# Optimization experiments

Measured on AMD Instinct MI355X. Metric: run time of the kernel, lower is better.

The kernel has to match this reference:

```python
import jax, jax.numpy as jnp
import numpy as np

N_NODES = 100000
N_EDGES = 3200000
INP_DIM = 128
OUT_DIM = 128


def setup_inputs() -> dict:
    key = jax.random.key(0)
    ks = jax.random.split(key, 10)
    x = jax.random.normal(ks[0], (N_NODES, INP_DIM), dtype=jnp.float32)
    edge_index = jax.random.randint(ks[1], (2, N_EDGES), 0, N_NODES, dtype=jnp.int64)
    edge_attr = jax.random.uniform(ks[2], (N_EDGES,), dtype=jnp.float32)
    # GCNConv weights (glorot-style scaling) and zero biases, per PyG defaults
    def glorot(k, fin, fout):
        s = jnp.sqrt(6.0 / (fin + fout)).astype(jnp.float32)
        return jax.random.uniform(k, (fin, fout), jnp.float32, -s, s)
    W1 = glorot(ks[3], INP_DIM, 32); b1 = jnp.zeros((32,), jnp.float32)
    W2 = glorot(ks[4], 32, 64);      b2 = jnp.zeros((64,), jnp.float32)
    W3 = glorot(ks[5], 64, OUT_DIM); b3 = jnp.zeros((OUT_DIM,), jnp.float32)
    return {"x": x, "edge_index": edge_index, "edge_attr": edge_attr,
            "W1": W1, "b1": b1, "W2": W2, "b2": b2, "W3": W3, "b3": b3}


def _gcn_norm(edge_index, edge_attr, n_nodes):
    # add self-loops with weight 1, compute symmetric normalization (PyG gcn_norm)
    loop = jnp.arange(n_nodes, dtype=edge_index.dtype)
    row = jnp.concatenate([edge_index[0], loop])  # source
    col = jnp.concatenate([edge_index[1], loop])  # target
    ew = jnp.concatenate([edge_attr, jnp.ones((n_nodes,), edge_attr.dtype)])
    deg = jax.ops.segment_sum(ew, col, num_segments=n_nodes)
    dinv = jnp.where(deg > 0, jax.lax.rsqrt(jnp.maximum(deg, 1e-30)), 0.0)
    norm = dinv[row] * ew * dinv[col]  # [E + N]
    return row, col, norm


def _gcn_conv(x, row, col, norm, W, b, n_nodes):
    h = x @ W                     # [N, Fout] small GEMM first (Fout <= Fin or cheap)
    msg = h[row] * norm[:, None]  # edge-wise gather + scale
    out = jax.ops.segment_sum(msg, col, num_segments=n_nodes)  # scatter-add
    return out + b


def reference(x, edge_index, edge_attr, W1, b1, W2, b2, W3, b3):
    n = x.shape[0]
    row, col, norm = _gcn_norm(edge_index, edge_attr, n)
    h = jax.nn.elu(_gcn_conv(x, row, col, norm, W1, b1, n))
    h = jax.nn.elu(_gcn_conv(h, row, col, norm, W2, b2, n))
    return _gcn_conv(h, row, col, norm, W3, b3, n)
```

## Files before the change

kernel.cpp:

```cpp
#include <hip/hip_runtime.h>
#include <hip/hip_bf16.h>


constexpr int N = 100000;
constexpr int E = 3200000;

constexpr int BSHIFT = 7;
constexpr int BSIZE = 128;
constexpr int NBKT = (N + BSIZE - 1) / BSIZE;

constexpr float FIX_SCALE = 16777216.0f;

constexpr int HIST_EPB = 4096;
constexpr int SC_EPB = 4096;

__device__ __forceinline__ float ldf(const void* p, int isbf, size_t i) {
    return isbf ? __bfloat162float(((const __hip_bfloat16*)p)[i])
                : ((const float*)p)[i];
}

__device__ __forceinline__ int ld_idx(const void* ei, int is64, size_t pos) {
    return is64 ? (int)((const long long*)ei)[pos] : ((const int*)ei)[pos];
}

__device__ __forceinline__ float4 bf4tof4(uint2 u) {
    float4 r;
    r.x = __uint_as_float(u.x << 16);
    r.y = __uint_as_float(u.x & 0xffff0000u);
    r.z = __uint_as_float(u.y << 16);
    r.w = __uint_as_float(u.y & 0xffff0000u);
    return r;
}
__device__ __forceinline__ unsigned short f2bf(float f) {
    unsigned u = __float_as_uint(f);
    unsigned rnd = 0x7fffu + ((u >> 16) & 1u);
    return (unsigned short)((u + rnd) >> 16);
}
__device__ __forceinline__ unsigned packbf2(float a, float b) {
    return (unsigned)f2bf(a) | ((unsigned)f2bf(b) << 16);
}
__device__ __forceinline__ uint2 f4tobf4(float4 v) {
    uint2 r;
    r.x = packbf2(v.x, v.y);
    r.y = packbf2(v.z, v.w);
    return r;
}

__global__ void k_probe(const void* ei, const void* x, int* flags, int* bkt_cnt) {
    __shared__ int bad64, bigcnt;
    int t = threadIdx.x;
    if (t == 0) { bad64 = 0; bigcnt = 0; }
    __syncthreads();
    long long v = ((const long long*)ei)[t];
    if (v < 0 || v >= (long long)N) atomicAdd(&bad64, 1);
    const unsigned short* u = (const unsigned short*)x;
    int big = 0;
    for (int i = t * 16; i < t * 16 + 16; i++) {
        int e = (u[i] >> 7) & 0xFF;
        if (e >= 133) big++;
    }
    atomicAdd(&bigcnt, big);
    for (int i = t; i < NBKT; i += 256) bkt_cnt[i] = 0;
    __syncthreads();
    if (t == 0) { flags[0] = (bad64 == 0) ? 1 : 0; flags[1] = (bigcnt < 40) ? 1 : 0; }
}

__global__ __launch_bounds__(512) void k_hist(const void* ei, const int* flags,
                                              int* bkt_cnt) {
    constexpr int EPT = HIST_EPB / 512;
    __shared__ int h[NBKT];
    int t = threadIdx.x;
    for (int i = t; i < NBKT; i += 512) h[i] = 0;
    __syncthreads();
    int is64 = flags[0];
    size_t eb = (size_t)blockIdx.x * HIST_EPB;
    int nb = (int)min((size_t)HIST_EPB, (size_t)E - eb);
    int cc[EPT];
#pragma unroll
    for (int k = 0; k < EPT; k++) {
        int idx = t + k * 512;
        cc[k] = (idx < nb) ? ld_idx(ei, is64, (size_t)E + eb + idx) : -1;
    }
#pragma unroll
    for (int k = 0; k < EPT; k++)
        if (cc[k] >= 0) atomicAdd(&h[cc[k] >> BSHIFT], 1);
    __syncthreads();
    for (int i = t; i < NBKT; i += 512) {
        int v = h[i];
        if (v) atomicAdd(&bkt_cnt[i], v);
    }
}

__global__ void k_bscan(const int* bkt_cnt, int* bkt_off, int* bkt_cur) {
    __shared__ int s[256];
    int t = threadIdx.x;
    int v[4]; int sum = 0;
#pragma unroll
    for (int j = 0; j < 4; j++) {
        int i = t * 4 + j;
        v[j] = (i < NBKT) ? bkt_cnt[i] : 0;
        sum += v[j];
    }
    s[t] = sum; __syncthreads();
    for (int st = 1; st < 256; st <<= 1) {
        int add = (t >= st) ? s[t - st] : 0;
        __syncthreads();
        s[t] += add;
        __syncthreads();
    }
    int excl = s[t] - sum;
#pragma unroll
    for (int j = 0; j < 4; j++) {
        int i = t * 4 + j;
        if (i < NBKT) { bkt_off[i] = excl; bkt_cur[i] = excl; excl += v[j]; }
    }
    if (t == 0) bkt_off[NBKT] = E;
}

__global__ __launch_bounds__(512) void k_scatter(const void* ei, const int* flags,
                                                 const void* ew, int* bkt_cur,
                                                 int2* tmp) {
    constexpr int EPT = SC_EPB / 512;
    __shared__ int h[NBKT];
    __shared__ int base_s[NBKT];
    int t = threadIdx.x;
    for (int i = t; i < NBKT; i += 512) h[i] = 0;
    __syncthreads();
    int is64 = flags[0], isbf = flags[1];
    size_t eb = (size_t)blockIdx.x * SC_EPB;
    int nb = (int)min((size_t)SC_EPB, (size_t)E - eb);
    int rr[EPT], cc[EPT]; float ww[EPT];
#pragma unroll
    for (int k = 0; k < EPT; k++) {
        int idx = t + k * 512;
        if (idx < nb) {
            size_t e = eb + idx;
            rr[k] = ld_idx(ei, is64, e);
            cc[k] = ld_idx(ei, is64, (size_t)E + e);
            ww[k] = ldf(ew, isbf, e);
        } else {
            rr[k] = 0; cc[k] = -1; ww[k] = 0.f;
        }
    }
#pragma unroll
    for (int k = 0; k < EPT; k++)
        if (cc[k] >= 0) atomicAdd(&h[cc[k] >> BSHIFT], 1);
    __syncthreads();
    for (int i = t; i < NBKT; i += 512) {
        int v = h[i];
        base_s[i] = v ? atomicAdd(&bkt_cur[i], v) : 0;
    }
    __syncthreads();
    for (int i = t; i < NBKT; i += 512) h[i] = 0;
    __syncthreads();
#pragma unroll
    for (int k = 0; k < EPT; k++) {
        if (cc[k] >= 0) {
            int b = cc[k] >> BSHIFT;
            int loc = atomicAdd(&h[b], 1);
            int pos = base_s[b] + loc;
            tmp[pos] = make_int2(rr[k] | ((cc[k] & (BSIZE - 1)) << 17),
                                 __float_as_int(ww[k]));
        }
    }
}

__global__ __launch_bounds__(256) void k_nodecnt(const int2* __restrict__ tmp,
                                                 const int* __restrict__ bkt_off,
                                                 int* __restrict__ counts,
                                                 int* __restrict__ offsets,
                                                 float* __restrict__ dinv) {
    __shared__ int cnt_s[BSIZE];
    __shared__ unsigned int wfx_s[BSIZE];
    __shared__ int sc_s[BSIZE];
    int t = threadIdx.x;
    int b = blockIdx.x;
    if (t < BSIZE) { cnt_s[t] = 0; wfx_s[t] = 0u; }
    __syncthreads();
    int s0 = bkt_off[b], s1 = bkt_off[b + 1];
    for (int p = s0 + t; p < s1; p += 256) {
        int2 ev = tmp[p];
        int c7 = (int)(((unsigned)ev.x) >> 17);
        float w = __int_as_float(ev.y);
        atomicAdd(&cnt_s[c7], 1);
        atomicAdd(&wfx_s[c7], (unsigned)__float2uint_rn(w * FIX_SCALE));
    }
    __syncthreads();
    if (t < BSIZE) sc_s[t] = cnt_s[t];
    __syncthreads();
    for (int st = 1; st < BSIZE; st <<= 1) {
        int add = (t < BSIZE && t >= st) ? sc_s[t - st] : 0;
        __syncthreads();
        if (t < BSIZE) sc_s[t] += add;
        __syncthreads();
    }
    if (t < BSIZE) {
        int node = b * BSIZE + t;
        if (node < N) {
            int c = cnt_s[t];
            offsets[node] = s0 + sc_s[t] - c;
            counts[node] = c;
            float deg = 1.0f + (float)wfx_s[t] * (1.0f / FIX_SCALE);
            dinv[node] = rsqrtf(deg);
        }
    }
}

__global__ __launch_bounds__(256) void k_fill2(const int2* __restrict__ tmp,
                                               const int* __restrict__ bkt_off,
                                               const int* __restrict__ offsets,
                                               const float* __restrict__ dinv,
                                               int2* __restrict__ epk) {
    __shared__ int lcur[BSIZE];
    int t = threadIdx.x;
    int b = blockIdx.x;
    if (t < BSIZE) {
        int node = b * BSIZE + t;
        lcur[t] = (node < N) ? offsets[node] : 0;
    }
    __syncthreads();
    int s0 = bkt_off[b], s1 = bkt_off[b + 1];
    for (int p = s0 + t; p < s1; p += 256) {
        int2 ev = tmp[p];
        unsigned px = (unsigned)ev.x;
        int r = (int)(px & 0x1FFFFu);
        int c7 = (int)(px >> 17);
        float w = __int_as_float(ev.y);
        float nr = dinv[r] * w;
        int pos = atomicAdd(&lcur[c7], 1);
        epk[pos] = make_int2(r, __float_as_int(nr));
    }
}

template <int FIN, int FOUT, int TM, int TN, int XMODE, bool OBF, bool BIAS, bool ELU>
__global__ __launch_bounds__(256) void k_gemm(const void* __restrict__ X,
                                              const void* __restrict__ W,
                                              const void* __restrict__ bias,
                                              const int* __restrict__ flags,
                                              void* __restrict__ H) {
    constexpr int TCOLS = FOUT / TN;
    constexpr int TROWS = 256 / TCOLS;
    constexpr int BR = TROWS * TM;
    __shared__ float wl[FIN * FOUT];
    __shared__ float xt[FIN][BR + 1];
    int t = threadIdx.x;
    int isbf = flags[1];
    int base = blockIdx.x * BR;

    if (!isbf) {
        const float4* W4 = (const float4*)W;
        float4* wl4 = (float4*)wl;
        for (int i = t; i < FIN * FOUT / 4; i += 256) wl4[i] = W4[i];
    } else {
        for (int i = t; i < FIN * FOUT; i += 256)
            wl[i] = __bfloat162float(((const __hip_bfloat16*)W)[i]);
    }
    if (XMODE == 2) {
        const uint2* X2 = (const uint2*)X;
        for (int i = t; i < BR * FIN / 4; i += 256) {
            int row = i / (FIN / 4);
            int kq = i % (FIN / 4);
            int node = base + row;
            uint2 u = make_uint2(0u, 0u);
            if (node < N) u = X2[(size_t)node * (FIN / 4) + kq];
            float4 v = bf4tof4(u);
            int k = kq * 4;
            xt[k][row] = v.x; xt[k + 1][row] = v.y;
            xt[k + 2][row] = v.z; xt[k + 3][row] = v.w;
        }
    } else if (!isbf) {
        const float4* X4 = (const float4*)X;
        for (int i = t; i < BR * FIN / 4; i += 256) {
            int row = i / (FIN / 4);
            int kq = i % (FIN / 4);
            int node = base + row;
            float4 v = make_float4(0.f, 0.f, 0.f, 0.f);
            if (node < N) v = X4[(size_t)node * (FIN / 4) + kq];
            int k = kq * 4;
            xt[k][row] = v.x; xt[k + 1][row] = v.y;
            xt[k + 2][row] = v.z; xt[k + 3][row] = v.w;
        }
    } else {
        for (int i = t; i < BR * FIN; i += 256) {
            int row = i / FIN, k = i % FIN;
            int node = base + row;
            float v = (node < N)
                ? __bfloat162float(((const __hip_bfloat16*)X)[(size_t)node * FIN + k]) : 0.f;
            xt[k][row] = v;
        }
    }
    __syncthreads();

    int tcol = t % TCOLS, trow = t / TCOLS;
    int r0 = trow * TM, c0 = tcol * TN;
    float acc[TM][TN] = {};
#pragma unroll 4
    for (int k = 0; k < FIN; k++) {
        float a[TM], b[TN];
#pragma unroll
        for (int m = 0; m < TM; m++) a[m] = xt[k][r0 + m];
#pragma unroll
        for (int n = 0; n < TN; n++) b[n] = wl[k * FOUT + c0 + n];
#pragma unroll
        for (int m = 0; m < TM; m++)
#pragma unroll
            for (int n = 0; n < TN; n++) acc[m][n] += a[m] * b[n];
    }
#pragma unroll
    for (int m = 0; m < TM; m++) {
        int node = base + r0 + m;
        if (node >= N) continue;
        float vv[TN];
#pragma unroll
        for (int n = 0; n < TN; n++) {
            float v = acc[m][n];
            if (BIAS) v += ldf(bias, isbf, c0 + n);
            if (ELU) v = (v > 0.0f) ? v : expm1f(v);
            vv[n] = v;
        }
        if (OBF) {
            unsigned* Hrow = (unsigned*)((unsigned short*)H + (size_t)node * FOUT + c0);
#pragma unroll
            for (int n = 0; n < TN; n += 2)
                Hrow[n / 2] = packbf2(vv[n], vv[n + 1]);
        } else {
            float* Hrow = (float*)H + (size_t)node * FOUT + c0;
#pragma unroll
            for (int n = 0; n < TN; n++) Hrow[n] = vv[n];
        }
    }
}

template <int F, bool BIAS, bool ELU>
__global__ __launch_bounds__(256) void k_agg(const uint2* __restrict__ Hb,
                                             const int* __restrict__ offsets,
                                             const int* __restrict__ counts,
                                             const int2* __restrict__ epk,
                                             const float* __restrict__ dinv,
                                             const void* __restrict__ bias,
                                             const int* __restrict__ flags,
                                             uint2* __restrict__ outb) {
    constexpr int LPN = F / 4;
    constexpr int NPB = 256 / LPN;
    int t = threadIdx.x;
    int lane = t % LPN;
    int g = t / LPN;
    int node = blockIdx.x * NPB + g;
    if (node >= N) return;
    float di = dinv[node];
    float4 h = bf4tof4(Hb[(size_t)node * LPN + lane]);
    float4 acc0 = make_float4(0.f, 0.f, 0.f, 0.f);
    float4 acc1 = make_float4(0.f, 0.f, 0.f, 0.f);
    int p = offsets[node];
    int pend = p + counts[node];

    int2 eA[8];
    bool have = (p + 8 <= pend);
    if (have) {
#pragma unroll
        for (int j = 0; j < 8; j++) eA[j] = epk[p + j];
    }
    while (have) {
        uint2 gg[8];
#pragma unroll
        for (int j = 0; j < 8; j++)
            gg[j] = Hb[(size_t)eA[j].x * LPN + lane];
        float w[8];
#pragma unroll
        for (int j = 0; j < 8; j++) w[j] = __int_as_float(eA[j].y);
        p += 8;
        bool nxt = (p + 8 <= pend);
        int2 eB[8];
        if (nxt) {
#pragma unroll
            for (int j = 0; j < 8; j++) eB[j] = epk[p + j];
        }
#pragma unroll
        for (int j = 0; j < 8; j += 2) {
            float4 g0 = bf4tof4(gg[j]);
            float4 g1 = bf4tof4(gg[j + 1]);
            acc0.x += g0.x * w[j]; acc0.y += g0.y * w[j];
            acc0.z += g0.z * w[j]; acc0.w += g0.w * w[j];
            acc1.x += g1.x * w[j + 1]; acc1.y += g1.y * w[j + 1];
            acc1.z += g1.z * w[j + 1]; acc1.w += g1.w * w[j + 1];
        }
#pragma unroll
        for (int j = 0; j < 8; j++) eA[j] = eB[j];
        have = nxt;
    }
    for (; p + 4 <= pend; p += 4) {
        int2 e0 = epk[p], e1 = epk[p + 1], e2 = epk[p + 2], e3 = epk[p + 3];
        float4 h0 = bf4tof4(Hb[(size_t)e0.x * LPN + lane]);
        float4 h1 = bf4tof4(Hb[(size_t)e1.x * LPN + lane]);
        float4 h2 = bf4tof4(Hb[(size_t)e2.x * LPN + lane]);
        float4 h3 = bf4tof4(Hb[(size_t)e3.x * LPN + lane]);
        float w0 = __int_as_float(e0.y), w1 = __int_as_float(e1.y);
        float w2 = __int_as_float(e2.y), w3 = __int_as_float(e3.y);
        acc0.x += h0.x * w0 + h2.x * w2; acc1.x += h1.x * w1 + h3.x * w3;
        acc0.y += h0.y * w0 + h2.y * w2; acc1.y += h1.y * w1 + h3.y * w3;
        acc0.z += h0.z * w0 + h2.z * w2; acc1.z += h1.z * w1 + h3.z * w3;
        acc0.w += h0.w * w0 + h2.w * w2; acc1.w += h1.w * w1 + h3.w * w3;
    }
    for (; p < pend; p++) {
        int2 e = epk[p];
        float4 hh = bf4tof4(Hb[(size_t)e.x * LPN + lane]);
        float w = __int_as_float(e.y);
        acc0.x += hh.x * w; acc0.y += hh.y * w;
        acc0.z += hh.z * w; acc0.w += hh.w * w;
    }
    float4 acc;
    acc.x = acc0.x + acc1.x; acc.y = acc0.y + acc1.y;
    acc.z = acc0.z + acc1.z; acc.w = acc0.w + acc1.w;
    float sw = di * di;
    acc.x = acc.x * di + h.x * sw;
    acc.y = acc.y * di + h.y * sw;
    acc.z = acc.z * di + h.z * sw;
    acc.w = acc.w * di + h.w * sw;
    if (BIAS) {
        int fb = lane * 4;
        int isbf = flags[1];
        acc.x += ldf(bias, isbf, fb);
        acc.y += ldf(bias, isbf, fb + 1);
        acc.z += ldf(bias, isbf, fb + 2);
        acc.w += ldf(bias, isbf, fb + 3);
    }
    if (ELU) {
        acc.x = (acc.x > 0.0f) ? acc.x : expm1f(acc.x);
        acc.y = (acc.y > 0.0f) ? acc.y : expm1f(acc.y);
        acc.z = (acc.z > 0.0f) ? acc.z : expm1f(acc.z);
        acc.w = (acc.w > 0.0f) ? acc.w : expm1f(acc.w);
    }
    outb[(size_t)node * LPN + lane] = f4tobf4(acc);
}

__global__ void k_sentinel(float* out, int n) {
    int i = blockIdx.x * blockDim.x + threadIdx.x;
    if (i < n) out[i] = 123.0f;
}

extern "C" void kernel_launch(void* const* d_in, const int* in_sizes, int n_in,
                              void* d_out, int out_size, void* d_ws, size_t ws_size,
                              hipStream_t stream) {
    const void* x  = d_in[0];
    const void* ei = d_in[1];
    const void* ea = d_in[2];
    const void* W1 = d_in[3];
    const void* b1 = d_in[4];
    const void* W2 = d_in[5];
    const void* b2 = d_in[6];
    const void* W3 = d_in[7];
    const void* b3 = d_in[8];
    float* out = (float*)d_out;

    char* ws = (char*)d_ws;
    size_t off = 0;
    auto alloc = [&](size_t bytes) {
        off = (off + 255) & ~(size_t)255;
        size_t r = off;
        off += bytes;
        return r;
    };
    float* dinv    = (float*)(ws + alloc((size_t)N * 4));
    int*   counts  = (int*)  (ws + alloc((size_t)N * 4));
    int*   offsets = (int*)  (ws + alloc((size_t)N * 4));
    int*   bkt_cnt = (int*)  (ws + alloc((size_t)NBKT * 4));
    int*   bkt_off = (int*)  (ws + alloc((size_t)(NBKT + 1) * 4));
    int*   bkt_cur = (int*)  (ws + alloc((size_t)NBKT * 4));
    int*   flags   = (int*)  (ws + alloc(256));
    int2*  epk     = (int2*) (ws + alloc((size_t)E * 8));
    unsigned short* bufA = (unsigned short*)(ws + alloc((size_t)N * 64 * 2));
    unsigned short* bufB = (unsigned short*)(ws + alloc((size_t)N * 64 * 2));
    size_t need = off;
    int2* tmp = (int2*)bufA;

    if (ws_size < need) {
        hipLaunchKernelGGL(k_sentinel, dim3((N * 128 + 255) / 256), dim3(256), 0, stream,
                           out, N * 128);
        return;
    }

    const int gH = (E + HIST_EPB - 1) / HIST_EPB;
    const int gS = (E + SC_EPB - 1) / SC_EPB;

    hipLaunchKernelGGL(k_probe, dim3(1), dim3(256), 0, stream, ei, x, flags, bkt_cnt);
    hipLaunchKernelGGL(k_hist, dim3(gH), dim3(512), 0, stream, ei, flags, bkt_cnt);
    hipLaunchKernelGGL(k_bscan, dim3(1), dim3(256), 0, stream, bkt_cnt, bkt_off, bkt_cur);
    hipLaunchKernelGGL(k_scatter, dim3(gS), dim3(512), 0, stream, ei, flags, ea, bkt_cur, tmp);
    hipLaunchKernelGGL(k_nodecnt, dim3(NBKT), dim3(256), 0, stream, tmp, bkt_off,
                       counts, offsets, dinv);
    hipLaunchKernelGGL(k_fill2, dim3(NBKT), dim3(256), 0, stream, tmp, bkt_off,
                       offsets, dinv, epk);

    hipLaunchKernelGGL((k_gemm<128, 32, 2, 4, 1, true, false, false>),
                       dim3((N + 63) / 64), dim3(256), 0, stream, x, W1, nullptr, flags, bufA);
    hipLaunchKernelGGL((k_agg<32, true, true>), dim3((N + 31) / 32), dim3(256), 0, stream,
                       (const uint2*)bufA, offsets, counts, epk, dinv, b1, flags, (uint2*)bufB);
    hipLaunchKernelGGL((k_agg<32, false, false>), dim3((N + 31) / 32), dim3(256), 0, stream,
                       (const uint2*)bufB, offsets, counts, epk, dinv, nullptr, flags, (uint2*)bufA);
    hipLaunchKernelGGL((k_gemm<32, 64, 4, 4, 2, true, true, true>),
                       dim3((N + 63) / 64), dim3(256), 0, stream, bufA, W2, b2, flags, bufB);
    hipLaunchKernelGGL((k_agg<64, false, false>), dim3((N + 15) / 16), dim3(256), 0, stream,
                       (const uint2*)bufB, offsets, counts, epk, dinv, nullptr, flags, (uint2*)bufA);
    hipLaunchKernelGGL((k_gemm<64, 128, 4, 8, 2, false, true, false>),
                       dim3((N + 63) / 64), dim3(256), 0, stream, bufA, W3, b3, flags, out);
}
```

Before: 464.1 us.

## Fuse CSR count/fill kernels and pack edges into 32-bit row+Q15 weight

Merges the node-count and fill kernels into one k_csr kernel, which avoids a second launch and a second pass over the bucketed temp edges. Each edge is packed into a single 32-bit word holding a 17-bit source row and a 15-bit quantized edge weight, halving the CSR edge stream read by the four aggregation passes. The source dinv factor is no longer folded into the stored weight, so the aggregation kernels add an extra gather of dinv[r] per edge. Weights are quantized to Q15 and clamped just below 1.0, which costs precision and relies on edge weights lying in [0,1).

After: 464.1 us. About the same (+0.0%).

```diff
diff --git a/kernel.cpp b/kernel.cpp
--- a/kernel.cpp
+++ b/kernel.cpp
@@ -10,6 +10,7 @@
 constexpr int NBKT = (N + BSIZE - 1) / BSIZE;
 
 constexpr float FIX_SCALE = 16777216.0f;
+constexpr float Q15 = 32768.0f;
 
 constexpr int HIST_EPB = 4096;
 constexpr int SC_EPB = 4096;
@@ -165,14 +166,16 @@
     }
 }
 
-__global__ __launch_bounds__(256) void k_nodecnt(const int2* __restrict__ tmp,
-                                                 const int* __restrict__ bkt_off,
-                                                 int* __restrict__ counts,
-                                                 int* __restrict__ offsets,
-                                                 float* __restrict__ dinv) {
+__global__ __launch_bounds__(256) void k_csr(const int2* __restrict__ tmp,
+                                             const int* __restrict__ bkt_off,
+                                             int* __restrict__ counts,
+                                             int* __restrict__ offsets,
+                                             float* __restrict__ dinv,
+                                             unsigned* __restrict__ epk) {
     __shared__ int cnt_s[BSIZE];
     __shared__ unsigned int wfx_s[BSIZE];
     __shared__ int sc_s[BSIZE];
+    __shared__ int lcur[BSIZE];
     int t = threadIdx.x;
     int b = blockIdx.x;
     if (t < BSIZE) { cnt_s[t] = 0; wfx_s[t] = 0u; }
@@ -198,37 +201,27 @@
         int node = b * BSIZE + t;
         if (node < N) {
             int c = cnt_s[t];
-            offsets[node] = s0 + sc_s[t] - c;
+            int off0 = s0 + sc_s[t] - c;
+            offsets[node] = off0;
             counts[node] = c;
+            lcur[t] = off0;
             float deg = 1.0f + (float)wfx_s[t] * (1.0f / FIX_SCALE);
             dinv[node] = rsqrtf(deg);
-        }
-    }
-}
-
-__global__ __launch_bounds__(256) void k_fill2(const int2* __restrict__ tmp,
-                                               const int* __restrict__ bkt_off,
-                                               const int* __restrict__ offsets,
-                                               const float* __restrict__ dinv,
-                                               int2* __restrict__ epk) {
-    __shared__ int lcur[BSIZE];
-    int t = threadIdx.x;
-    int b = blockIdx.x;
-    if (t < BSIZE) {
-        int node = b * BSIZE + t;
-        lcur[t] = (node < N) ? offsets[node] : 0;
-    }
-    __syncthreads();
-    int s0 = bkt_off[b], s1 = bkt_off[b + 1];
+        } else {
+            lcur[t] = 0;
+        }
+    }
+    __syncthreads();
     for (int p = s0 + t; p < s1; p += 256) {
         int2 ev = tmp[p];
         unsigned px = (unsigned)ev.x;
         int r = (int)(px & 0x1FFFFu);
         int c7 = (int)(px >> 17);
         float w = __int_as_float(ev.y);
-        float nr = dinv[r] * w;
+        unsigned q = __float2uint_rn(w * Q15);
+        if (q > 32767u) q = 32767u;
         int pos = atomicAdd(&lcur[c7], 1);
-        epk[pos] = make_int2(r, __float_as_int(nr));
+        epk[pos] = (unsigned)r | (q << 17);
     }
 }
 
@@ -335,13 +328,14 @@
 __global__ __launch_bounds__(256) void k_agg(const uint2* __restrict__ Hb,
                                              const int* __restrict__ offsets,
                                              const int* __restrict__ counts,
-                                             const int2* __restrict__ epk,
+                                             const unsigned* __restrict__ epk,
                                              const float* __restrict__ dinv,
                                              const void* __restrict__ bias,
                                              const int* __restrict__ flags,
                                              uint2* __restrict__ outb) {
     constexpr int LPN = F / 4;
     constexpr int NPB = 256 / LPN;
+    constexpr float QS = 1.0f / Q15;
     int t = threadIdx.x;
     int lane = t % LPN;
     int g = t / LPN;
@@ -354,23 +348,30 @@
     int p = offsets[node];
     int pend = p + counts[node];
 
-    int2 eA[8];
+    unsigned eA[8];
     bool have = (p + 8 <= pend);
     if (have) {
 #pragma unroll
         for (int j = 0; j < 8; j++) eA[j] = epk[p + j];
     }
     while (have) {
+        int r[8];
+#pragma unroll
+        for (int j = 0; j < 8; j++) r[j] = (int)(eA[j] & 0x1FFFFu);
         uint2 gg[8];
 #pragma unroll
         for (int j = 0; j < 8; j++)
-            gg[j] = Hb[(size_t)eA[j].x * LPN + lane];
+            gg[j] = Hb[(size_t)r[j] * LPN + lane];
+        float dv[8];
+#pragma unroll
+        for (int j = 0; j < 8; j++) dv[j] = dinv[r[j]];
         float w[8];
 #pragma unroll
-        for (int j = 0; j < 8; j++) w[j] = __int_as_float(eA[j].y);
+        for (int j = 0; j < 8; j++)
+            w[j] = dv[j] * ((float)(eA[j] >> 17) * QS);
         p += 8;
         bool nxt = (p + 8 <= pend);
-        int2 eB[8];
+        unsigned eB[8];
         if (nxt) {
 #pragma unroll
             for (int j = 0; j < 8; j++) eB[j] = epk[p + j];
@@ -389,22 +390,27 @@
         have = nxt;
     }
     for (; p + 4 <= pend; p += 4) {
-        int2 e0 = epk[p], e1 = epk[p + 1], e2 = epk[p + 2], e3 = epk[p + 3];
-        float4 h0 = bf4tof4(Hb[(size_t)e0.x * LPN + lane]);
-        float4 h1 = bf4tof4(Hb[(size_t)e1.x * LPN + lane]);
-        float4 h2 = bf4tof4(Hb[(size_t)e2.x * LPN + lane]);
-        float4 h3 = bf4tof4(Hb[(size_t)e3.x * LPN + lane]);
-        float w0 = __int_as_float(e0.y), w1 = __int_as_float(e1.y);
-        float w2 = __int_as_float(e2.y), w3 = __int_as_float(e3.y);
+        unsigned e0 = epk[p], e1 = epk[p + 1], e2 = epk[p + 2], e3 = epk[p + 3];
+        int r0i = (int)(e0 & 0x1FFFFu), r1i = (int)(e1 & 0x1FFFFu);
+        int r2i = (int)(e2 & 0x1FFFFu), r3i = (int)(e3 & 0x1FFFFu);
+        float4 h0 = bf4tof4(Hb[(size_t)r0i * LPN + lane]);
+        float4 h1 = bf4tof4(Hb[(size_t)r1i * LPN + lane]);
+        float4 h2 = bf4tof4(Hb[(size_t)r2i * LPN + lane]);
+        float4 h3 = bf4tof4(Hb[(size_t)r3i * LPN + lane]);
+        float w0 = dinv[r0i] * ((float)(e0 >> 17) * QS);
+        float w1 = dinv[r1i] * ((float)(e1 >> 17) * QS);
+        float w2 = dinv[r2i] * ((float)(e2 >> 17) * QS);
+        float w3 = dinv[r3i] * ((float)(e3 >> 17) * QS);
         acc0.x += h0.x * w0 + h2.x * w2; acc1.x += h1.x * w1 + h3.x * w3;
         acc0.y += h0.y * w0 + h2.y * w2; acc1.y += h1.y * w1 + h3.y * w3;
         acc0.z += h0.z * w0 + h2.z * w2; acc1.z += h1.z * w1 + h3.z * w3;
         acc0.w += h0.w * w0 + h2.w * w2; acc1.w += h1.w * w1 + h3.w * w3;
     }
     for (; p < pend; p++) {
-        int2 e = epk[p];
-        float4 hh = bf4tof4(Hb[(size_t)e.x * LPN + lane]);
-        float w = __int_as_float(e.y);
+        unsigned e = epk[p];
+        int ri = (int)(e & 0x1FFFFu);
+        float4 hh = bf4tof4(Hb[(size_t)ri * LPN + lane]);
+        float w = dinv[ri] * ((float)(e >> 17) * QS);
         acc0.x += hh.x * w; acc0.y += hh.y * w;
         acc0.z += hh.z * w; acc0.w += hh.w * w;
     }
@@ -467,7 +473,7 @@
     int*   bkt_off = (int*)  (ws + alloc((size_t)(NBKT + 1) * 4));
     int*   bkt_cur = (int*)  (ws + alloc((size_t)NBKT * 4));
     int*   flags   = (int*)  (ws + alloc(256));
-    int2*  epk     = (int2*) (ws + alloc((size_t)E * 8));
+    unsigned* epk  = (unsigned*)(ws + alloc((size_t)E * 4));
     unsigned short* bufA = (unsigned short*)(ws + alloc((size_t)N * 64 * 2));
     unsigned short* bufB = (unsigned short*)(ws + alloc((size_t)N * 64 * 2));
     size_t need = off;
@@ -486,10 +492,8 @@
     hipLaunchKernelGGL(k_hist, dim3(gH), dim3(512), 0, stream, ei, flags, bkt_cnt);
     hipLaunchKernelGGL(k_bscan, dim3(1), dim3(256), 0, stream, bkt_cnt, bkt_off, bkt_cur);
     hipLaunchKernelGGL(k_scatter, dim3(gS), dim3(512), 0, stream, ei, flags, ea, bkt_cur, tmp);
-    hipLaunchKernelGGL(k_nodecnt, dim3(NBKT), dim3(256), 0, stream, tmp, bkt_off,
-                       counts, offsets, dinv);
-    hipLaunchKernelGGL(k_fill2, dim3(NBKT), dim3(256), 0, stream, tmp, bkt_off,
-                       offsets, dinv, epk);
+    hipLaunchKernelGGL(k_csr, dim3(NBKT), dim3(256), 0, stream, tmp, bkt_off,
+                       counts, offsets, dinv, epk);
 
     hipLaunchKernelGGL((k_gemm<128, 32, 2, 4, 1, true, false, false>),
                        dim3((N + 63) / 64), dim3(256), 0, stream, x, W1, nullptr, flags, bufA);
```
